# Optimization experiments

Hardware: AMD Instinct MI355X
Metric: run time of the kernel (lower is better)

## Reference

```python
import jax, jax.numpy as jnp
import numpy as np
import math

B, S, D = 2, 1024, 2048
NH, NKV, HD = 16, 8, 128
NREP = NH // NKV
WINDOW = 256  # = max_seq_len; ReRoPE window


def _rope(x, cos, sin):
    # x: (b, s, h, d); cos/sin broadcastable to (b, s, h, d//2). Interleaved pairs (llama2.c style).
    b, s, h, d = x.shape
    xr, xi = x[..., ::2], x[..., 1::2]
    or_ = xr * cos - xi * sin
    oi = xr * sin + xi * cos
    return jnp.stack([or_, oi], axis=-1).reshape(b, s, h, d)


def setup_inputs() -> dict:
    key = jax.random.key(0)
    kx, kq, kk, kv, ko = jax.random.split(key, 5)
    # real RoPE tables (theta=10000), per-position, half head dim
    inv = 1.0 / (10000.0 ** (np.arange(0, HD, 2, dtype=np.float32) / HD))
    fr = np.outer(np.arange(S, dtype=np.float32), inv).astype(np.float32)  # (S, HD//2)
    sc = 0.02
    return {
        "x": jax.random.normal(kx, (B, S, D), jnp.float32),
        "freqs_cos": jnp.asarray(np.cos(fr)),
        "freqs_sin": jnp.asarray(np.sin(fr)),
        "wq": jax.random.normal(kq, (D, NH * HD), jnp.float32) * sc,
        "wk": jax.random.normal(kk, (D, NKV * HD), jnp.float32) * sc,
        "wv": jax.random.normal(kv, (D, NKV * HD), jnp.float32) * sc,
        "wo": jax.random.normal(ko, (NH * HD, D), jnp.float32) * sc,
    }


def reference(x, freqs_cos, freqs_sin, wq, wk, wv, wo):
    b, s, _ = x.shape
    xq = (x @ wq).reshape(b, s, NH, HD)
    xk = (x @ wk).reshape(b, s, NKV, HD)
    xv = (x @ wv).reshape(b, s, NKV, HD)

    cos = freqs_cos[:s][None, :, None, :]
    sin = freqs_sin[:s][None, :, None, :]
    q1 = _rope(xq, cos, sin)   # standard RoPE
    k1 = _rope(xk, cos, sin)

    # ReRoPE: queries rotated at the fixed clamp position = window; keys unrotated
    cw = freqs_cos[WINDOW][None, None, None, :]
    sw = freqs_sin[WINDOW][None, None, None, :]
    q2 = _rope(xq, cw, sw)
    k2 = xk

    rep = lambda a: jnp.repeat(a, NREP, axis=2)          # repeat_kv (GQA)
    heads = lambda a: a.transpose(0, 2, 1, 3)            # (b, h, s, d)
    q1, k1, v = heads(q1), heads(rep(k1)), heads(rep(xv))
    q2, k2 = heads(q2), heads(rep(k2))

    scale = 1.0 / math.sqrt(HD)
    s1 = jnp.einsum("bhqd,bhkd->bhqk", q1, k1) * scale
    s2 = jnp.einsum("bhqd,bhkd->bhqk", q2, k2) * scale

    i = jnp.arange(s)[:, None]
    j = jnp.arange(s)[None, :]
    causal = j <= i
    rect = causal & (j > i - WINDOW)                     # rectified_mask band
    scores = jnp.where(rect, s1, s2)
    scores = jnp.where(causal, scores, -jnp.inf)         # mask_inf (causal)

    attn = jax.nn.softmax(scores.astype(jnp.float32), axis=-1).astype(x.dtype)
    out = jnp.einsum("bhqk,bhkd->bhqd", attn, v)
    out = out.transpose(0, 2, 1, 3).reshape(b, s, NH * HD)
    return out @ wo
```

## Files before the change

### kernel.cpp

```cpp
#include <hip/hip_runtime.h>
#include <hip/hip_bf16.h>

#define BDIM 2
#define SDIM 1024
#define DDIM 2048
#define NH 16
#define NKV 8
#define HD 128
#define WINDOW 256

typedef __bf16 bf16;
typedef __bf16 bf16x4 __attribute__((ext_vector_type(4)));
typedef __bf16 bf16x8 __attribute__((ext_vector_type(8)));
typedef float f32x4 __attribute__((ext_vector_type(4)));

#define L2E 1.44269504088896341f

__device__ inline bf16x8 load8(const bf16* p) { return *reinterpret_cast<const bf16x8*>(p); }

__device__ __forceinline__ void gl_lds16(const bf16* g, bf16* l) {
  __builtin_amdgcn_global_load_lds(
      (__attribute__((address_space(1))) void*)g,
      (__attribute__((address_space(3))) void*)l,
      16, 0, 0);
}

__global__ __launch_bounds__(256) void cast_f32_bf16(const float* __restrict__ src,
                                                     bf16* __restrict__ dst) {
  long i = ((long)blockIdx.x * 256 + threadIdx.x) * 8;
  float4 a = *(const float4*)(src + i);
  float4 b = *(const float4*)(src + i + 4);
  bf16x8 o;
  o[0] = (bf16)a.x; o[1] = (bf16)a.y; o[2] = (bf16)a.z; o[3] = (bf16)a.w;
  o[4] = (bf16)b.x; o[5] = (bf16)b.y; o[6] = (bf16)b.z; o[7] = (bf16)b.w;
  *(bf16x8*)(dst + i) = o;
}

__global__ __launch_bounds__(256) void wtrans_all(const float* __restrict__ wq,
                                                  const float* __restrict__ wk,
                                                  const float* __restrict__ wv,
                                                  const float* __restrict__ wo,
                                                  bf16* __restrict__ wqkvT,
                                                  bf16* __restrict__ woT) {
  __shared__ bf16 tile[32][33];
  int z = blockIdx.z;
  const float* src; bf16* dst; int C;
  if (z == 0)      { src = wq; dst = wqkvT;                 C = 2048; }
  else if (z == 1) { src = wk; dst = wqkvT + 2048L * 2048;  C = 1024; }
  else if (z == 2) { src = wv; dst = wqkvT + 3072L * 2048;  C = 1024; }
  else             { src = wo; dst = woT;                   C = 2048; }
  int c0 = blockIdx.x * 32, r0 = blockIdx.y * 32;
  if (c0 >= C) return;
  int x = threadIdx.x, y = threadIdx.y;
  for (int yy = y; yy < 32; yy += 8)
    tile[yy][x] = (bf16)src[(long)(r0 + yy) * C + c0 + x];
  __syncthreads();
  for (int yy = y; yy < 32; yy += 8)
    dst[(long)(c0 + yy) * 2048 + r0 + x] = tile[x][yy];
}

#define BK 64
__global__ __launch_bounds__(256) void gemm_bt_n64(const bf16* __restrict__ A,
                                                   const bf16* __restrict__ Bt,
                                                   float* __restrict__ C,
                                                   int M, int N, int K) {
  __shared__ bf16 As[128 * BK];
  __shared__ bf16 Bs[64 * BK];
  int m0 = blockIdx.y * 128, n0 = blockIdx.x * 64;
  int t = threadIdx.x;
  int wid = t >> 6, lane = t & 63;
  int wm = (wid >> 1) * 64, wn = (wid & 1) * 32;
  int fm = lane & 15, quad = lane >> 4;
  f32x4 acc[4][2] = {};
  for (int k0 = 0; k0 < K; k0 += BK) {
    for (int p = 0; p < 4; ++p) {
      int idx = p * 256 + t;
      int row = idx >> 3, ccs = idx & 7;
      int gcol = ((ccs ^ (row & 7)) * 8);
      gl_lds16(&A[(long)(m0 + row) * K + k0 + gcol], &As[idx * 8]);
    }
    for (int p = 0; p < 2; ++p) {
      int idx = p * 256 + t;
      int row = idx >> 3, ccs = idx & 7;
      int gcol = ((ccs ^ (row & 7)) * 8);
      gl_lds16(&Bt[(long)(n0 + row) * K + k0 + gcol], &Bs[idx * 8]);
    }
    __syncthreads();
    for (int ks = 0; ks < BK; ks += 32) {
      int cc = (ks >> 3) + quad;
      bf16x8 af[4], bfr[2];
      for (int i = 0; i < 4; ++i) {
        int fr = wm + i * 16 + fm;
        af[i] = load8(&As[(fr * 8 + (cc ^ (fr & 7))) * 8]);
      }
      for (int j = 0; j < 2; ++j) {
        int fr = wn + j * 16 + fm;
        bfr[j] = load8(&Bs[(fr * 8 + (cc ^ (fr & 7))) * 8]);
      }
      for (int i = 0; i < 4; ++i)
        for (int j = 0; j < 2; ++j)
          acc[i][j] = __builtin_amdgcn_mfma_f32_16x16x32_bf16(af[i], bfr[j], acc[i][j], 0, 0, 0);
    }
    __syncthreads();
  }
  for (int i = 0; i < 4; ++i)
    for (int r = 0; r < 4; ++r) {
      int row = m0 + wm + i * 16 + quad * 4 + r;
      for (int j = 0; j < 2; ++j) {
        int col = n0 + wn + j * 16 + fm;
        C[(long)row * N + col] = acc[i][j][r];
      }
    }
}

#define VPITCH 130
__global__ __launch_bounds__(256) void gemm_qkv(const bf16* __restrict__ A,
                                                const bf16* __restrict__ Bt,
                                                const float* __restrict__ fc,
                                                const float* __restrict__ fs,
                                                bf16* __restrict__ q1,
                                                bf16* __restrict__ q2,
                                                bf16* __restrict__ k1,
                                                bf16* __restrict__ k2,
                                                bf16* __restrict__ vT) {
  const int K = 2048;
  __shared__ bf16 smem[128 * VPITCH];
  bf16* As = smem;
  bf16* Bs = smem + 8192;
  int m0 = blockIdx.y * 128, n0 = blockIdx.x * 128;
  int t = threadIdx.x;
  int wid = t >> 6, lane = t & 63;
  int wm = (wid >> 1) * 64, wn = (wid & 1) * 64;
  int fm = lane & 15, quad = lane >> 4;
  f32x4 acc[4][4] = {};
  for (int k0 = 0; k0 < K; k0 += BK) {
    for (int p = 0; p < 4; ++p) {
      int idx = p * 256 + t;
      int row = idx >> 3, ccs = idx & 7;
      int gcol = ((ccs ^ (row & 7)) * 8);
      gl_lds16(&A[(long)(m0 + row) * K + k0 + gcol], &As[idx * 8]);
      gl_lds16(&Bt[(long)(n0 + row) * K + k0 + gcol], &Bs[idx * 8]);
    }
    __syncthreads();
    for (int ks = 0; ks < BK; ks += 32) {
      int cc = (ks >> 3) + quad;
      bf16x8 af[4], bfr[4];
      for (int i = 0; i < 4; ++i) {
        int fr = wm + i * 16 + fm;
        af[i] = load8(&As[(fr * 8 + (cc ^ (fr & 7))) * 8]);
      }
      for (int i = 0; i < 4; ++i) {
        int fr = wn + i * 16 + fm;
        bfr[i] = load8(&Bs[(fr * 8 + (cc ^ (fr & 7))) * 8]);
      }
      for (int i = 0; i < 4; ++i)
        for (int j = 0; j < 4; ++j)
          acc[i][j] = __builtin_amdgcn_mfma_f32_16x16x32_bf16(af[i], bfr[j], acc[i][j], 0, 0, 0);
    }
    __syncthreads();
  }

  int n0h = n0 >> 7;
  float sgn = (lane & 1) ? 1.f : -1.f;
  if (n0h < 16) {
    const float scale = 0.08838834764831845f;
    float cwj[4], swj[4];
    for (int j = 0; j < 4; ++j) {
      int dp = (wn + j * 16 + fm) >> 1;
      cwj[j] = fc[WINDOW * 64 + dp];
      swj[j] = fs[WINDOW * 64 + dp] * sgn;
    }
    for (int i = 0; i < 4; ++i)
      for (int r = 0; r < 4; ++r) {
        int row = m0 + wm + i * 16 + quad * 4 + r;
        int s = row & (SDIM - 1);
        for (int j = 0; j < 4; ++j) {
          int col = wn + j * 16 + fm;
          int dp = col >> 1;
          float v = acc[i][j][r];
          float pp = __shfl_xor(v, 1, 64);
          float c = fc[s * 64 + dp];
          float sn = fs[s * 64 + dp] * sgn;
          long dst = (long)row * 2048 + n0h * 128 + col;
          q1[dst] = (bf16)((v * c + pp * sn) * scale);
          q2[dst] = (bf16)((v * cwj[j] + pp * swj[j]) * scale);
        }
      }
  } else if (n0h < 24) {
    int kvh = n0h - 16;
    for (int i = 0; i < 4; ++i)
      for (int r = 0; r < 4; ++r) {
        int row = m0 + wm + i * 16 + quad * 4 + r;
        int s = row & (SDIM - 1);
        for (int j = 0; j < 4; ++j) {
          int col = wn + j * 16 + fm;
          int dp = col >> 1;
          float v = acc[i][j][r];
          float pp = __shfl_xor(v, 1, 64);
          float c = fc[s * 64 + dp];
          float sn = fs[s * 64 + dp] * sgn;
          long dst = (long)row * 1024 + kvh * 128 + col;
          k1[dst] = (bf16)(v * c + pp * sn);
          k2[dst] = (bf16)v;
        }
      }
  } else {
    int vv = n0h - 24;
    for (int i = 0; i < 4; ++i)
      for (int j = 0; j < 4; ++j) {
        int col = wn + j * 16 + fm;
        for (int r = 0; r < 4; ++r) {
          int rl = wm + i * 16 + quad * 4 + r;
          smem[col * VPITCH + rl] = (bf16)acc[i][j][r];
        }
      }
    __syncthreads();
    int s0l = m0 & (SDIM - 1);
    int bq = m0 >> 10;
    bf16* vtg = vT + ((long)(bq * NKV + vv)) * 128 * 1024;
    for (int p = 0; p < 8; ++p) {
      int c = p * 256 + t;
      int d = c >> 4, sc = (c & 15) * 8;
      *(bf16x8*)&vtg[(long)d * 1024 + s0l + sc] = *(bf16x8*)&smem[d * VPITCH + sc];
    }
  }
}

__global__ __launch_bounds__(256) void attn_kernel(const bf16* __restrict__ q1,
                                                   const bf16* __restrict__ q2,
                                                   const bf16* __restrict__ k1,
                                                   const bf16* __restrict__ k2,
                                                   const bf16* __restrict__ vT,
                                                   bf16* __restrict__ aout) {
  __shared__ bf16 Ks[16384];
  __shared__ bf16 VTs[8192];
  __shared__ bf16 Pl[4][16][72];
  __shared__ float stats[4][16];

  int h = blockIdx.y;
  int b = blockIdx.z;
  int tile = b ? (15 - blockIdx.x) : blockIdx.x;
  int kv = h >> 1;
  int t = threadIdx.x;
  int w = t >> 6, lane = t & 63;
  int m = lane & 15, quad = lane >> 4;

  const bf16* k1g0 = k1 + ((long)b * SDIM) * 1024 + kv * 128;
  const bf16* k2g0 = k2 + ((long)b * SDIM) * 1024 + kv * 128;
  const bf16* vtg0 = vT + ((long)(b * NKV + kv)) * 128 * 1024;

  int t0 = tile * 64;
  int i0w = t0 + w * 16;

  const bf16* q1p = q1 + ((long)(b * SDIM + i0w + m)) * 2048 + h * 128 + quad * 8;
  const bf16* q2p = q2 + ((long)(b * SDIM + i0w + m)) * 2048 + h * 128 + quad * 8;
  bf16x8 q1f[4], q2f[4];
  for (int kc = 0; kc < 4; ++kc) {
    q1f[kc] = load8(q1p + kc * 32);
    q2f[kc] = load8(q2p + kc * 32);
  }

  f32x4 o[8] = {};
  float mrow = -INFINITY, lrow = 0.f;

  for (int j0 = 0; j0 < t0 + 64; j0 += 64) {
    bool c1 = (j0 + 63 > t0 - WINDOW);
    bool c2 = (j0 <= t0 + 63 - WINDOW);
    __syncthreads();
    for (int p = 0; p < 4; ++p) {
      int idx = p * 256 + t;
      int kr = idx >> 4, kcs = idx & 15;
      int kg = (kcs ^ (kr & 15)) * 8;
      if (c1) gl_lds16(&k1g0[(long)(j0 + kr) * 1024 + kg], &Ks[idx * 8]);
      if (c2) gl_lds16(&k2g0[(long)(j0 + kr) * 1024 + kg], &Ks[8192 + idx * 8]);
      int vd = idx >> 3, vcs = idx & 7;
      int vg = (vcs ^ (vd & 7)) * 8;
      gl_lds16(&vtg0[(long)vd * 1024 + j0 + vg], &VTs[idx * 8]);
    }
    __syncthreads();

    if (j0 < i0w + 16) {
      bool need1 = (j0 + 63 > i0w - WINDOW);
      bool need2 = (j0 <= i0w + 15 - WINDOW);
      f32x4 s1[4] = {}, s2[4] = {};
      if (need1)
        for (int st = 0; st < 4; ++st)
          for (int kc = 0; kc < 4; ++kc) {
            int cc = kc * 4 + quad;
            s1[st] = __builtin_amdgcn_mfma_f32_16x16x32_bf16(
                load8(&Ks[((st * 16 + m) * 16 + (cc ^ m)) * 8]), q1f[kc], s1[st], 0, 0, 0);
          }
      if (need2)
        for (int st = 0; st < 4; ++st)
          for (int kc = 0; kc < 4; ++kc) {
            int cc = kc * 4 + quad;
            s2[st] = __builtin_amdgcn_mfma_f32_16x16x32_bf16(
                load8(&Ks[8192 + ((st * 16 + m) * 16 + (cc ^ m)) * 8]), q2f[kc], s2[st], 0, 0, 0);
          }
      int i = i0w + m;
      float sv[4][4];
      for (int st = 0; st < 4; ++st)
        for (int r = 0; r < 4; ++r) {
          int j = j0 + st * 16 + quad * 4 + r;
          float v;
          if (j > i) v = -INFINITY;
          else if (j > i - WINDOW) v = s1[st][r];
          else v = s2[st][r];
          sv[st][r] = v;
        }
      float bm = -INFINITY;
      for (int st = 0; st < 4; ++st)
        for (int r = 0; r < 4; ++r) bm = fmaxf(bm, sv[st][r]);
      bm = fmaxf(bm, __shfl_xor(bm, 16, 64));
      bm = fmaxf(bm, __shfl_xor(bm, 32, 64));
      float mnew = fmaxf(mrow, bm);
      float alpha = exp2f((mrow - mnew) * L2E);
      float rs = 0.f;
      for (int st = 0; st < 4; ++st) {
        bf16x4 pk;
        for (int r = 0; r < 4; ++r) {
          float pvv = exp2f((sv[st][r] - mnew) * L2E);
          rs += pvv;
          pk[r] = (bf16)pvv;
        }
        *(bf16x4*)&Pl[w][m][st * 16 + quad * 4] = pk;
      }
      rs += __shfl_xor(rs, 16, 64);
      rs += __shfl_xor(rs, 32, 64);
      lrow = lrow * alpha + rs;
      mrow = mnew;
      if (lane < 16) stats[w][lane] = alpha;
      f32x4 av = *(f32x4*)&stats[w][quad * 4];
      for (int n8 = 0; n8 < 8; ++n8)
        for (int r = 0; r < 4; ++r) o[n8][r] *= av[r];
      for (int kc = 0; kc < 2; ++kc) {
        bf16x8 af = load8(&Pl[w][m][kc * 32 + quad * 8]);
        int cc = kc * 4 + quad;
        for (int n8 = 0; n8 < 8; ++n8) {
          int d = n8 * 16 + m;
          o[n8] = __builtin_amdgcn_mfma_f32_16x16x32_bf16(
              af, load8(&VTs[(d * 8 + (cc ^ (d & 7))) * 8]), o[n8], 0, 0, 0);
        }
      }
    }
  }

  if (lane < 16) stats[w][lane] = lrow;
  __builtin_amdgcn_s_waitcnt(0);
  f32x4 lv = *(f32x4*)&stats[w][quad * 4];
  for (int n8 = 0; n8 < 8; ++n8)
    for (int r = 0; r < 4; ++r) {
      int row = i0w + quad * 4 + r;
      float val = o[n8][r] / lv[r];
      aout[((long)(b * SDIM + row)) * 2048 + h * 128 + n8 * 16 + m] = (bf16)val;
    }
}

extern "C" void kernel_launch(void* const* d_in, const int* in_sizes, int n_in,
                              void* d_out, int out_size, void* d_ws, size_t ws_size,
                              hipStream_t stream) {
  const float* x  = (const float*)d_in[0];
  const float* fc = (const float*)d_in[1];
  const float* fs = (const float*)d_in[2];
  const float* wq = (const float*)d_in[3];
  const float* wk = (const float*)d_in[4];
  const float* wv = (const float*)d_in[5];
  const float* wo = (const float*)d_in[6];
  float* out = (float*)d_out;

  bf16* wqkvT = (bf16*)d_ws;
  bf16* woT   = wqkvT + 4096L * 2048;
  bf16* xb    = woT + 2048L * 2048;
  bf16* q1    = xb + 2048L * 2048;
  bf16* q2    = q1 + 2048L * 2048;
  bf16* k1b   = q2 + 2048L * 2048;
  bf16* k2b   = k1b + 2048L * 1024;
  bf16* vT    = k2b + 2048L * 1024;
  bf16* aout  = vT + 2048L * 1024;

  cast_f32_bf16<<<2048, 256, 0, stream>>>(x, xb);
  wtrans_all<<<dim3(64, 64, 4), dim3(32, 8), 0, stream>>>(wq, wk, wv, wo, wqkvT, woT);

  gemm_qkv<<<dim3(32, 16), 256, 0, stream>>>(xb, wqkvT, fc, fs, q1, q2, k1b, k2b, vT);

  attn_kernel<<<dim3(16, 16, 2), 256, 0, stream>>>(q1, q2, k1b, k2b, vT, aout);

  gemm_bt_n64<<<dim3(32, 16), 256, 0, stream>>>(aout, woT, out, 2048, 2048, 2048);
}
```

Before: 245.0 us.

## Move ReRoPE window rotation onto keys and apply query RoPE inside attention

Instead of materializing two rotated query tensors, the QKV GEMM now writes a single scaled, unrotated query tensor. The fixed-window inverse rotation is applied to the second key tensor instead. The attention kernel computes the standard RoPE query fragments on the fly from the cos/sin tables. This cuts global memory writes and reads of query data. Separately, the input cast and weight transpose kernels are merged into one launch. It adds per-block trig table loads and extra rounding order differences in attention.

```diff
diff --git a/kernel.cpp b/kernel.cpp
--- a/kernel.cpp
+++ b/kernel.cpp
@@ -25,25 +25,25 @@
       16, 0, 0);
 }
 
-__global__ __launch_bounds__(256) void cast_f32_bf16(const float* __restrict__ src,
-                                                     bf16* __restrict__ dst) {
-  long i = ((long)blockIdx.x * 256 + threadIdx.x) * 8;
-  float4 a = *(const float4*)(src + i);
-  float4 b = *(const float4*)(src + i + 4);
-  bf16x8 o;
-  o[0] = (bf16)a.x; o[1] = (bf16)a.y; o[2] = (bf16)a.z; o[3] = (bf16)a.w;
-  o[4] = (bf16)b.x; o[5] = (bf16)b.y; o[6] = (bf16)b.z; o[7] = (bf16)b.w;
-  *(bf16x8*)(dst + i) = o;
-}
-
-__global__ __launch_bounds__(256) void wtrans_all(const float* __restrict__ wq,
-                                                  const float* __restrict__ wk,
-                                                  const float* __restrict__ wv,
-                                                  const float* __restrict__ wo,
-                                                  bf16* __restrict__ wqkvT,
-                                                  bf16* __restrict__ woT) {
+__global__ __launch_bounds__(256) void prep(const float* __restrict__ x,
+                                            const float* __restrict__ wq,
+                                            const float* __restrict__ wk,
+                                            const float* __restrict__ wv,
+                                            const float* __restrict__ wo,
+                                            bf16* __restrict__ xb,
+                                            bf16* __restrict__ wqkvT,
+                                            bf16* __restrict__ woT) {
   __shared__ bf16 tile[32][33];
   int z = blockIdx.z;
+  int tx = threadIdx.x, ty = threadIdx.y;
+  if (z == 4) {
+    long i = (((long)blockIdx.y * 64 + blockIdx.x) * 256 + ty * 32 + tx) * 4;
+    float4 a = *(const float4*)(x + i);
+    bf16x4 o;
+    o[0] = (bf16)a.x; o[1] = (bf16)a.y; o[2] = (bf16)a.z; o[3] = (bf16)a.w;
+    *(bf16x4*)(xb + i) = o;
+    return;
+  }
   const float* src; bf16* dst; int C;
   if (z == 0)      { src = wq; dst = wqkvT;                 C = 2048; }
   else if (z == 1) { src = wk; dst = wqkvT + 2048L * 2048;  C = 1024; }
@@ -51,12 +51,11 @@
   else             { src = wo; dst = woT;                   C = 2048; }
   int c0 = blockIdx.x * 32, r0 = blockIdx.y * 32;
   if (c0 >= C) return;
-  int x = threadIdx.x, y = threadIdx.y;
-  for (int yy = y; yy < 32; yy += 8)
-    tile[yy][x] = (bf16)src[(long)(r0 + yy) * C + c0 + x];
+  for (int yy = ty; yy < 32; yy += 8)
+    tile[yy][tx] = (bf16)src[(long)(r0 + yy) * C + c0 + tx];
   __syncthreads();
-  for (int yy = y; yy < 32; yy += 8)
-    dst[(long)(c0 + yy) * 2048 + r0 + x] = tile[x][yy];
+  for (int yy = ty; yy < 32; yy += 8)
+    dst[(long)(c0 + yy) * 2048 + r0 + tx] = tile[tx][yy];
 }
 
 #define BK 64
@@ -118,8 +117,7 @@
                                                 const bf16* __restrict__ Bt,
                                                 const float* __restrict__ fc,
                                                 const float* __restrict__ fs,
-                                                bf16* __restrict__ q1,
-                                                bf16* __restrict__ q2,
+                                                bf16* __restrict__ q0,
                                                 bf16* __restrict__ k1,
                                                 bf16* __restrict__ k2,
                                                 bf16* __restrict__ vT) {
@@ -161,33 +159,25 @@
   }
 
   int n0h = n0 >> 7;
-  float sgn = (lane & 1) ? 1.f : -1.f;
   if (n0h < 16) {
     const float scale = 0.08838834764831845f;
+    for (int i = 0; i < 4; ++i)
+      for (int r = 0; r < 4; ++r) {
+        int row = m0 + wm + i * 16 + quad * 4 + r;
+        for (int j = 0; j < 4; ++j) {
+          int col = wn + j * 16 + fm;
+          q0[(long)row * 2048 + n0h * 128 + col] = (bf16)(acc[i][j][r] * scale);
+        }
+      }
+  } else if (n0h < 24) {
+    int kvh = n0h - 16;
+    float sgn = (lane & 1) ? 1.f : -1.f;
     float cwj[4], swj[4];
     for (int j = 0; j < 4; ++j) {
       int dp = (wn + j * 16 + fm) >> 1;
       cwj[j] = fc[WINDOW * 64 + dp];
-      swj[j] = fs[WINDOW * 64 + dp] * sgn;
-    }
-    for (int i = 0; i < 4; ++i)
-      for (int r = 0; r < 4; ++r) {
-        int row = m0 + wm + i * 16 + quad * 4 + r;
-        int s = row & (SDIM - 1);
-        for (int j = 0; j < 4; ++j) {
-          int col = wn + j * 16 + fm;
-          int dp = col >> 1;
-          float v = acc[i][j][r];
-          float pp = __shfl_xor(v, 1, 64);
-          float c = fc[s * 64 + dp];
-          float sn = fs[s * 64 + dp] * sgn;
-          long dst = (long)row * 2048 + n0h * 128 + col;
-          q1[dst] = (bf16)((v * c + pp * sn) * scale);
-          q2[dst] = (bf16)((v * cwj[j] + pp * swj[j]) * scale);
-        }
-      }
-  } else if (n0h < 24) {
-    int kvh = n0h - 16;
+      swj[j] = fs[WINDOW * 64 + dp] * (-sgn);
+    }
     for (int i = 0; i < 4; ++i)
       for (int r = 0; r < 4; ++r) {
         int row = m0 + wm + i * 16 + quad * 4 + r;
@@ -201,7 +191,7 @@
           float sn = fs[s * 64 + dp] * sgn;
           long dst = (long)row * 1024 + kvh * 128 + col;
           k1[dst] = (bf16)(v * c + pp * sn);
-          k2[dst] = (bf16)v;
+          k2[dst] = (bf16)(v * cwj[j] + pp * swj[j]);
         }
       }
   } else {
@@ -226,11 +216,12 @@
   }
 }
 
-__global__ __launch_bounds__(256) void attn_kernel(const bf16* __restrict__ q1,
-                                                   const bf16* __restrict__ q2,
+__global__ __launch_bounds__(256) void attn_kernel(const bf16* __restrict__ q0,
                                                    const bf16* __restrict__ k1,
                                                    const bf16* __restrict__ k2,
                                                    const bf16* __restrict__ vT,
+                                                   const float* __restrict__ fc,
+                                                   const float* __restrict__ fs,
                                                    bf16* __restrict__ aout) {
   __shared__ bf16 Ks[16384];
   __shared__ bf16 VTs[8192];
@@ -252,12 +243,18 @@
   int t0 = tile * 64;
   int i0w = t0 + w * 16;
 
-  const bf16* q1p = q1 + ((long)(b * SDIM + i0w + m)) * 2048 + h * 128 + quad * 8;
-  const bf16* q2p = q2 + ((long)(b * SDIM + i0w + m)) * 2048 + h * 128 + quad * 8;
-  bf16x8 q1f[4], q2f[4];
+  const bf16* q0p = q0 + ((long)(b * SDIM + i0w + m)) * 2048 + h * 128 + quad * 8;
+  bf16x8 q0f[4], q1f[4];
+  int srow = i0w + m;
   for (int kc = 0; kc < 4; ++kc) {
-    q1f[kc] = load8(q1p + kc * 32);
-    q2f[kc] = load8(q2p + kc * 32);
+    q0f[kc] = load8(q0p + kc * 32);
+    for (int p4 = 0; p4 < 4; ++p4) {
+      int dp = kc * 16 + quad * 4 + p4;
+      float c = fc[srow * 64 + dp], sn = fs[srow * 64 + dp];
+      float xr = (float)q0f[kc][2 * p4], xi = (float)q0f[kc][2 * p4 + 1];
+      q1f[kc][2 * p4]     = (bf16)(xr * c - xi * sn);
+      q1f[kc][2 * p4 + 1] = (bf16)(xr * sn + xi * c);
+    }
   }
 
   f32x4 o[8] = {};
@@ -295,7 +292,7 @@
           for (int kc = 0; kc < 4; ++kc) {
             int cc = kc * 4 + quad;
             s2[st] = __builtin_amdgcn_mfma_f32_16x16x32_bf16(
-                load8(&Ks[8192 + ((st * 16 + m) * 16 + (cc ^ m)) * 8]), q2f[kc], s2[st], 0, 0, 0);
+                load8(&Ks[8192 + ((st * 16 + m) * 16 + (cc ^ m)) * 8]), q0f[kc], s2[st], 0, 0, 0);
           }
       int i = i0w + m;
       float sv[4][4];
@@ -371,19 +368,17 @@
   bf16* wqkvT = (bf16*)d_ws;
   bf16* woT   = wqkvT + 4096L * 2048;
   bf16* xb    = woT + 2048L * 2048;
-  bf16* q1    = xb + 2048L * 2048;
-  bf16* q2    = q1 + 2048L * 2048;
-  bf16* k1b   = q2 + 2048L * 2048;
+  bf16* q0b   = xb + 2048L * 2048;
+  bf16* k1b   = q0b + 2048L * 2048;
   bf16* k2b   = k1b + 2048L * 1024;
   bf16* vT    = k2b + 2048L * 1024;
   bf16* aout  = vT + 2048L * 1024;
 
-  cast_f32_bf16<<<2048, 256, 0, stream>>>(x, xb);
-  wtrans_all<<<dim3(64, 64, 4), dim3(32, 8), 0, stream>>>(wq, wk, wv, wo, wqkvT, woT);
-
-  gemm_qkv<<<dim3(32, 16), 256, 0, stream>>>(xb, wqkvT, fc, fs, q1, q2, k1b, k2b, vT);
-
-  attn_kernel<<<dim3(16, 16, 2), 256, 0, stream>>>(q1, q2, k1b, k2b, vT, aout);
+  prep<<<dim3(64, 64, 5), dim3(32, 8), 0, stream>>>(x, wq, wk, wv, wo, xb, wqkvT, woT);
+
+  gemm_qkv<<<dim3(32, 16), 256, 0, stream>>>(xb, wqkvT, fc, fs, q0b, k1b, k2b, vT);
+
+  attn_kernel<<<dim3(16, 16, 2), 256, 0, stream>>>(q0b, k1b, k2b, vT, fc, fs, aout);
 
   gemm_bt_n64<<<dim3(32, 16), 256, 0, stream>>>(aout, woT, out, 2048, 2048, 2048);
 }
```

Result: no change. 243.1 us (-0.8%).
